# Performance work log

Hardware: AMD Instinct MI355X
Metric: run time of the kernel (lower is better)

Reference implementation:

```python
import jax, jax.numpy as jnp
import numpy as np

B, S, D, H, E, F = 4, 2048, 1024, 16, 8, 4096
CAP_FACTOR = 1.25
DH = D // H


def setup_inputs() -> dict:
    key = jax.random.key(0)
    ks = jax.random.split(key, 8)
    s = 0.02
    return {
        "src": jax.random.normal(ks[0], (B, S, D), jnp.float32),
        "src_pad_mask": jnp.zeros((B, S), jnp.bool_),  # True = padding
        "ln1_g": jnp.ones((D,), jnp.float32),
        "ln1_b": jnp.zeros((D,), jnp.float32),
        "in_proj_w": jax.random.normal(ks[1], (3 * D, D), jnp.float32) * s,
        "in_proj_b": jnp.zeros((3 * D,), jnp.float32),
        "out_proj_w": jax.random.normal(ks[2], (D, D), jnp.float32) * s,
        "out_proj_b": jnp.zeros((D,), jnp.float32),
        "ln2_g": jnp.ones((D,), jnp.float32),
        "ln2_b": jnp.zeros((D,), jnp.float32),
        "router_w": jax.random.normal(ks[3], (D, E), jnp.float32) * s,
        "router_b": jnp.zeros((E,), jnp.float32),
        "w1": jax.random.normal(ks[4], (E, D, F), jnp.float32) * s,
        "b1": jnp.zeros((E, F), jnp.float32),
        "w2": jax.random.normal(ks[5], (E, F, D), jnp.float32) * s,
        "b2": jnp.zeros((E, D), jnp.float32),
    }


def _layernorm(x, g, b, eps=1e-5):
    m = jnp.mean(x, axis=-1, keepdims=True)
    v = jnp.mean(jnp.square(x - m), axis=-1, keepdims=True)
    return (x - m) * jax.lax.rsqrt(v + eps) * g + b


def _mha(x, pad_mask, in_proj_w, in_proj_b, out_proj_w, out_proj_b):
    qkv = x @ in_proj_w.T + in_proj_b                      # [B,S,3D]
    q, k, v = jnp.split(qkv, 3, axis=-1)
    q = q.reshape(B, S, H, DH)
    k = k.reshape(B, S, H, DH)
    v = v.reshape(B, S, H, DH)
    scores = jnp.einsum('bqhd,bkhd->bhqk', q, k) / np.sqrt(DH).astype(np.float32)
    scores = jnp.where(pad_mask[:, None, None, :], jnp.float32(-1e9), scores)
    attn = jax.nn.softmax(scores, axis=-1)
    out = jnp.einsum('bhqk,bkhd->bqhd', attn, v).reshape(B, S, D)
    return out @ out_proj_w.T + out_proj_b


def _switch(x, token_mask, router_w, router_b, w1, b1, w2, b2):
    N = B * S
    cap = int(CAP_FACTOR * N / E)
    tokens = x.reshape(N, D)
    tm = token_mask.reshape(N).astype(jnp.float32)
    logits = tokens @ router_w + router_b                  # [N,E]
    probs = jax.nn.softmax(logits, axis=-1)
    eidx = jnp.argmax(probs, axis=-1)                      # [N] top-1 expert
    gate = jnp.take_along_axis(probs, eidx[:, None], axis=1)[:, 0]
    oh = jax.nn.one_hot(eidx, E, dtype=jnp.float32) * tm[:, None]
    # position of each token within its expert's queue (1-based; 0 if masked)
    pos = jnp.sum(jnp.cumsum(oh, axis=0) * oh, axis=-1)
    keep = (pos > 0) & (pos <= cap)
    slot = eidx * cap + (pos - 1).astype(jnp.int32)        # flat slot in [E*cap)
    slot_scatter = jnp.where(keep, slot, E * cap)          # out-of-range => dropped
    keepf = keep.astype(jnp.float32)
    dispatch = jnp.zeros((E * cap, D), jnp.float32).at[slot_scatter].set(
        tokens * keepf[:, None], mode='drop')
    d = dispatch.reshape(E, cap, D)
    h = jax.nn.relu(jnp.einsum('ecd,edf->ecf', d, w1) + b1[:, None, :])
    o = jnp.einsum('ecf,efd->ecd', h, w2) + b2[:, None, :]
    slot_gather = jnp.where(keep, slot, 0)
    out = o.reshape(E * cap, D)[slot_gather] * (gate * keepf)[:, None]
    # aux losses over valid tokens
    denom = jnp.maximum(jnp.sum(tm), 1.0)
    f = jnp.sum(oh, axis=0) / denom                        # dispatch fraction per expert
    P = jnp.sum(probs * tm[:, None], axis=0) / denom       # mean router prob per expert
    lb_loss = E * jnp.sum(f * P)
    z_loss = jnp.sum(jnp.square(jax.nn.logsumexp(logits, axis=-1)) * tm) / denom
    return out.reshape(B, S, D), lb_loss, z_loss


def reference(src, src_pad_mask, ln1_g, ln1_b, in_proj_w, in_proj_b,
              out_proj_w, out_proj_b, ln2_g, ln2_b, router_w, router_b,
              w1, b1, w2, b2):
    x = _layernorm(src, ln1_g, ln1_b)
    attn = _mha(x, src_pad_mask, in_proj_w, in_proj_b, out_proj_w, out_proj_b)
    src1 = src + attn                                      # dropout=0.0
    token_mask = ~src_pad_mask
    x2 = _layernorm(src1, ln2_g, ln2_b)
    ffn, lb_loss, z_loss = _switch(x2, token_mask, router_w, router_b, w1, b1, w2, b2)
    src2 = src1 + ffn
    return (src2, lb_loss, z_loss)
```

## Files before the change

kernel.cpp:

```cpp
#include <hip/hip_runtime.h>

constexpr int cB = 4, cS = 2048, cD = 1024, cH = 16, cE = 8, cF = 4096;
constexpr int cN = cB * cS;
constexpr int cDH = 64;
constexpr int cCAP = 1280;

typedef __attribute__((ext_vector_type(8))) short bf16x8;
typedef __attribute__((ext_vector_type(4))) float f32x4;
typedef __attribute__((ext_vector_type(4))) unsigned short u16x4;

__device__ inline unsigned short bf16_rne(float x) {
  unsigned u = __float_as_uint(x);
  u += 0x7FFF + ((u >> 16) & 1);
  return (unsigned short)(u >> 16);
}
__device__ inline float bf16_f(unsigned short h) {
  return __uint_as_float(((unsigned)h) << 16);
}

__global__ __launch_bounds__(256) void ln_kernel(const float* __restrict__ x,
                                                 const float* __restrict__ g,
                                                 const float* __restrict__ bb,
                                                 float* __restrict__ y) {
  __shared__ float red[8];
  const int row = blockIdx.x;
  const int t = threadIdx.x;
  const float4 v = ((const float4*)(x + (size_t)row * cD))[t];
  float s = v.x + v.y + v.z + v.w;
#pragma unroll
  for (int m = 32; m >= 1; m >>= 1) s += __shfl_xor(s, m, 64);
  if ((t & 63) == 0) red[t >> 6] = s;
  __syncthreads();
  const float mean = (red[0] + red[1] + red[2] + red[3]) * (1.0f / cD);
  const float dx = v.x - mean, dy = v.y - mean, dz = v.z - mean, dw = v.w - mean;
  float ss = dx * dx + dy * dy + dz * dz + dw * dw;
#pragma unroll
  for (int m = 32; m >= 1; m >>= 1) ss += __shfl_xor(ss, m, 64);
  if ((t & 63) == 0) red[4 + (t >> 6)] = ss;
  __syncthreads();
  const float var = (red[4] + red[5] + red[6] + red[7]) * (1.0f / cD);
  const float inv = rsqrtf(var + 1e-5f);
  const float4 gg = ((const float4*)g)[t];
  const float4 b4 = ((const float4*)bb)[t];
  float4 o;
  o.x = dx * inv * gg.x + b4.x;
  o.y = dy * inv * gg.y + b4.y;
  o.z = dz * inv * gg.z + b4.z;
  o.w = dw * inv * gg.w + b4.w;
  ((float4*)(y + (size_t)row * cD))[t] = o;
}

__global__ __launch_bounds__(256) void ln_split_kernel(
    const float* __restrict__ x, const float* __restrict__ g,
    const float* __restrict__ bb, unsigned short* __restrict__ yh,
    unsigned short* __restrict__ yl) {
  __shared__ float red[8];
  const int row = blockIdx.x;
  const int t = threadIdx.x;
  const float4 v = ((const float4*)(x + (size_t)row * cD))[t];
  float s = v.x + v.y + v.z + v.w;
#pragma unroll
  for (int m = 32; m >= 1; m >>= 1) s += __shfl_xor(s, m, 64);
  if ((t & 63) == 0) red[t >> 6] = s;
  __syncthreads();
  const float mean = (red[0] + red[1] + red[2] + red[3]) * (1.0f / cD);
  const float dx = v.x - mean, dy = v.y - mean, dz = v.z - mean, dw = v.w - mean;
  float ss = dx * dx + dy * dy + dz * dz + dw * dw;
#pragma unroll
  for (int m = 32; m >= 1; m >>= 1) ss += __shfl_xor(ss, m, 64);
  if ((t & 63) == 0) red[4 + (t >> 6)] = ss;
  __syncthreads();
  const float var = (red[4] + red[5] + red[6] + red[7]) * (1.0f / cD);
  const float inv = rsqrtf(var + 1e-5f);
  const float4 gg = ((const float4*)g)[t];
  const float4 b4 = ((const float4*)bb)[t];
  const float oa[4] = {dx * inv * gg.x + b4.x, dy * inv * gg.y + b4.y,
                       dz * inv * gg.z + b4.z, dw * inv * gg.w + b4.w};
  u16x4 hh, ll;
#pragma unroll
  for (int i = 0; i < 4; i++) {
    const unsigned short h16 = bf16_rne(oa[i]);
    hh[i] = h16;
    ll[i] = bf16_rne(oa[i] - bf16_f(h16));
  }
  *(u16x4*)(yh + (size_t)row * cD + t * 4) = hh;
  *(u16x4*)(yl + (size_t)row * cD + t * 4) = ll;
}

__global__ __launch_bounds__(256) void wsplit_kernel(const float* __restrict__ in,
                                                     unsigned short* __restrict__ hi,
                                                     unsigned short* __restrict__ lo,
                                                     int n4) {
  const int i = blockIdx.x * 256 + threadIdx.x;
  if (i >= n4) return;
  const float4 v = ((const float4*)in)[i];
  const float a[4] = {v.x, v.y, v.z, v.w};
  u16x4 hh, ll;
#pragma unroll
  for (int j = 0; j < 4; j++) {
    const unsigned short h16 = bf16_rne(a[j]);
    hh[j] = h16;
    ll[j] = bf16_rne(a[j] - bf16_f(h16));
  }
  *(u16x4*)(hi + (size_t)i * 4) = hh;
  *(u16x4*)(lo + (size_t)i * 4) = ll;
}

__global__ __launch_bounds__(256) void transpose_bf16_kernel(
    const float* __restrict__ in, unsigned short* __restrict__ outp, int Rr,
    int Cc) {
  __shared__ float T[64][65];
  const int z = blockIdx.z;
  in += (size_t)z * Rr * Cc;
  outp += (size_t)z * Rr * Cc;
  const int c0 = blockIdx.x * 64, r0 = blockIdx.y * 64;
  const int tid = threadIdx.x;
#pragma unroll
  for (int u = 0; u < 4; u++) {
    const int a = tid + u * 256;
    const int r = a >> 4, c4 = (a & 15) << 2;
    const float4 v = *(const float4*)(in + (size_t)(r0 + r) * Cc + c0 + c4);
    T[r][c4 + 0] = v.x;
    T[r][c4 + 1] = v.y;
    T[r][c4 + 2] = v.z;
    T[r][c4 + 3] = v.w;
  }
  __syncthreads();
#pragma unroll
  for (int u = 0; u < 4; u++) {
    const int a = tid + u * 256;
    const int c = a >> 4, r4 = (a & 15) << 2;
    u16x4 o;
#pragma unroll
    for (int i = 0; i < 4; i++) o[i] = bf16_rne(T[r4 + i][c]);
    *(u16x4*)(outp + (size_t)(c0 + c) * Rr + r0 + r4) = o;
  }
}

template <bool SPLIT, bool RELU, bool RESID, int OUT>
__global__ __launch_bounds__(256) void gemm_bf16(
    const unsigned short* __restrict__ Ah, const unsigned short* __restrict__ Al,
    size_t sA,
    const unsigned short* __restrict__ Bh, const unsigned short* __restrict__ Bl,
    size_t sB,
    const float* __restrict__ bias, size_t sBias,
    const float* __restrict__ R,
    void* __restrict__ Cv, size_t sC,
    int K, int lda, int ldb, int ldc,
    unsigned short* __restrict__ Qh, unsigned short* __restrict__ Ql,
    unsigned short* __restrict__ Kh, unsigned short* __restrict__ Kl,
    unsigned short* __restrict__ Vth, unsigned short* __restrict__ Vtl) {
  __shared__ unsigned short AsH[128 * 40];
  __shared__ unsigned short BsH[128 * 40];
  __shared__ unsigned short AsL[SPLIT ? 128 * 40 : 8];
  __shared__ unsigned short BsL[SPLIT ? 128 * 40 : 8];
  const int z = blockIdx.z;
  Ah += (size_t)z * sA;
  Bh += (size_t)z * sB;
  if constexpr (SPLIT) {
    Al += (size_t)z * sA;
    Bl += (size_t)z * sB;
  }
  bias += (size_t)z * sBias;
  const int n0 = blockIdx.x * 128, m0 = blockIdx.y * 128;
  const int tid = threadIdx.x;
  const int wid = tid >> 6, lane = tid & 63;
  const int ln = lane & 15, quad = lane >> 4;
  const int wm = (wid >> 1) * 64, wn = (wid & 1) * 64;

  f32x4 acc[4][4];
#pragma unroll
  for (int i = 0; i < 4; i++)
#pragma unroll
    for (int j = 0; j < 4; j++) acc[i][j] = (f32x4){0.f, 0.f, 0.f, 0.f};

  for (int k0 = 0; k0 < K; k0 += 32) {
    __syncthreads();
#pragma unroll
    for (int u = 0; u < 2; u++) {
      const int c = tid + u * 256;
      const int row = c >> 2, ko = (c & 3) << 3;
      const int ld = row * 40 + ko;
      *(uint4*)&AsH[ld] = *(const uint4*)(Ah + (size_t)(m0 + row) * lda + k0 + ko);
      *(uint4*)&BsH[ld] = *(const uint4*)(Bh + (size_t)(n0 + row) * ldb + k0 + ko);
      if constexpr (SPLIT) {
        *(uint4*)&AsL[ld] = *(const uint4*)(Al + (size_t)(m0 + row) * lda + k0 + ko);
        *(uint4*)&BsL[ld] = *(const uint4*)(Bl + (size_t)(n0 + row) * ldb + k0 + ko);
      }
    }
    __syncthreads();
    bf16x8 bh[4], bl[4];
#pragma unroll
    for (int nt = 0; nt < 4; nt++) {
      bh[nt] = *(const bf16x8*)&BsH[(wn + nt * 16 + ln) * 40 + quad * 8];
      if constexpr (SPLIT)
        bl[nt] = *(const bf16x8*)&BsL[(wn + nt * 16 + ln) * 40 + quad * 8];
    }
#pragma unroll
    for (int mt = 0; mt < 4; mt++) {
      const bf16x8 ah = *(const bf16x8*)&AsH[(wm + mt * 16 + ln) * 40 + quad * 8];
      bf16x8 al;
      if constexpr (SPLIT)
        al = *(const bf16x8*)&AsL[(wm + mt * 16 + ln) * 40 + quad * 8];
#pragma unroll
      for (int nt = 0; nt < 4; nt++) {
        acc[mt][nt] =
            __builtin_amdgcn_mfma_f32_16x16x32_bf16(ah, bh[nt], acc[mt][nt], 0, 0, 0);
        if constexpr (SPLIT) {
          acc[mt][nt] =
              __builtin_amdgcn_mfma_f32_16x16x32_bf16(al, bh[nt], acc[mt][nt], 0, 0, 0);
          acc[mt][nt] =
              __builtin_amdgcn_mfma_f32_16x16x32_bf16(ah, bl[nt], acc[mt][nt], 0, 0, 0);
        }
      }
    }
  }
  if constexpr (OUT == 2) {
#pragma unroll
    for (int mt = 0; mt < 4; mt++) {
      const int row0 = m0 + wm + mt * 16 + quad * 4;
      const int b_ = row0 >> 11, s0_ = row0 & 2047;
      const size_t bbase = (size_t)b_ * cH * cS * cDH;
#pragma unroll
      for (int nt = 0; nt < 4; nt++) {
        const int col = n0 + wn + nt * 16 + ln;
        const float bv = bias[col];
        const int sec = col >> 10;
        const int f = col & 1023;
        const int hh = f >> 6, d = f & 63;
        const size_t bh_off = bbase + (size_t)hh * cS * cDH;
        float vals[4];
#pragma unroll
        for (int r = 0; r < 4; r++) vals[r] = acc[mt][nt][r] + bv;
        if (sec == 2) {
          u16x4 hi4, lo4;
#pragma unroll
          for (int r = 0; r < 4; r++) {
            const unsigned short h16 = bf16_rne(vals[r]);
            hi4[r] = h16;
            lo4[r] = bf16_rne(vals[r] - bf16_f(h16));
          }
          const size_t idx = bh_off + (size_t)d * cS + s0_;
          *(u16x4*)(Vth + idx) = hi4;
          *(u16x4*)(Vtl + idx) = lo4;
        } else {
          unsigned short* dsth = (sec == 0) ? Qh : Kh;
          unsigned short* dstl = (sec == 0) ? Ql : Kl;
#pragma unroll
          for (int r = 0; r < 4; r++) {
            const unsigned short h16 = bf16_rne(vals[r]);
            const size_t idx = bh_off + (size_t)(s0_ + r) * cDH + d;
            dsth[idx] = h16;
            dstl[idx] = bf16_rne(vals[r] - bf16_f(h16));
          }
        }
      }
    }
  } else {
    float* Cf = nullptr;
    unsigned short* Cb = nullptr;
    if constexpr (OUT == 1)
      Cb = (unsigned short*)Cv + (size_t)z * sC;
    else
      Cf = (float*)Cv + (size_t)z * sC;
#pragma unroll
    for (int mt = 0; mt < 4; mt++) {
#pragma unroll
      for (int nt = 0; nt < 4; nt++) {
        const int col = n0 + wn + nt * 16 + ln;
        const float bv = bias[col];
#pragma unroll
        for (int r = 0; r < 4; r++) {
          const int row = m0 + wm + mt * 16 + quad * 4 + r;
          float v = acc[mt][nt][r] + bv;
          if constexpr (RELU) v = fmaxf(v, 0.f);
          if constexpr (RESID) v += R[(size_t)row * ldc + col];
          if constexpr (OUT == 1)
            Cb[(size_t)row * ldc + col] = bf16_rne(v);
          else
            Cf[(size_t)row * ldc + col] = v;
        }
      }
    }
  }
}

__global__ __launch_bounds__(256) void attn_mfma_kernel(
    const unsigned short* __restrict__ Qh, const unsigned short* __restrict__ Ql,
    const unsigned short* __restrict__ Kh, const unsigned short* __restrict__ Kl,
    const unsigned short* __restrict__ Vth, const unsigned short* __restrict__ Vtl,
    const unsigned char* __restrict__ pad, unsigned short* __restrict__ Oh,
    unsigned short* __restrict__ Ol) {
  __shared__ unsigned short KsH[64 * 72];
  __shared__ unsigned short KsL[64 * 72];
  __shared__ unsigned short VsH[64 * 72];
  __shared__ unsigned short VsL[64 * 72];
  __shared__ unsigned short PsH[4 * 16 * 72];
  __shared__ unsigned short PsL[4 * 16 * 72];
  __shared__ float Mk[64];

  const int q0 = blockIdx.x << 6;
  const int h = blockIdx.y, b = blockIdx.z;
  const int tid = threadIdx.x;
  const int wid = tid >> 6, lane = tid & 63;
  const int ln = lane & 15, quad = lane >> 4;
  constexpr float SC2 = 0.125f * 1.4426950408889634f;

  const size_t bh = (size_t)(b * cH + h);
  const unsigned short* gKh = Kh + bh * cS * cDH;
  const unsigned short* gKl = Kl + bh * cS * cDH;
  const unsigned short* gVh = Vth + bh * cDH * cS;
  const unsigned short* gVl = Vtl + bh * cDH * cS;

  const size_t qbase = (bh * cS + q0 + wid * 16 + ln) * cDH;
  bf16x8 qh[2], ql[2];
#pragma unroll
  for (int ks = 0; ks < 2; ks++) {
    qh[ks] = *(const bf16x8*)(Qh + qbase + ks * 32 + quad * 8);
    ql[ks] = *(const bf16x8*)(Ql + qbase + ks * 32 + quad * 8);
  }

  f32x4 Oc[4];
#pragma unroll
  for (int dt = 0; dt < 4; dt++) Oc[dt] = (f32x4){0.f, 0.f, 0.f, 0.f};
  float mprev = -1e30f, lrun = 0.f;

  for (int kt = 0; kt < cS / 64; kt++) {
    const int k0 = kt << 6;
    __syncthreads();
#pragma unroll
    for (int u = 0; u < 2; u++) {
      const int a = tid + (u << 8);
      const int row = a >> 3, c8 = (a & 7) << 3;
      const int ld = row * 72 + c8;
      *(uint4*)&KsH[ld] = *(const uint4*)(gKh + (size_t)(k0 + row) * cDH + c8);
      *(uint4*)&KsL[ld] = *(const uint4*)(gKl + (size_t)(k0 + row) * cDH + c8);
      *(uint4*)&VsH[ld] = *(const uint4*)(gVh + (size_t)row * cS + k0 + c8);
      *(uint4*)&VsL[ld] = *(const uint4*)(gVl + (size_t)row * cS + k0 + c8);
    }
    if (tid < 64) Mk[tid] = pad[b * cS + k0 + tid] ? -1e30f : 0.0f;
    __syncthreads();

    float sf[4][4];
#pragma unroll
    for (int st = 0; st < 4; st++) {
      f32x4 acc = (f32x4){0.f, 0.f, 0.f, 0.f};
      const unsigned short* krH = &KsH[(st * 16 + ln) * 72];
      const unsigned short* krL = &KsL[(st * 16 + ln) * 72];
#pragma unroll
      for (int ks = 0; ks < 2; ks++) {
        const bf16x8 kh = *(const bf16x8*)(krH + ks * 32 + quad * 8);
        const bf16x8 kl = *(const bf16x8*)(krL + ks * 32 + quad * 8);
        acc = __builtin_amdgcn_mfma_f32_16x16x32_bf16(kh, qh[ks], acc, 0, 0, 0);
        acc = __builtin_amdgcn_mfma_f32_16x16x32_bf16(kl, qh[ks], acc, 0, 0, 0);
        acc = __builtin_amdgcn_mfma_f32_16x16x32_bf16(kh, ql[ks], acc, 0, 0, 0);
      }
      const float4 mkv = *(const float4*)&Mk[st * 16 + quad * 4];
      sf[st][0] = acc[0] * SC2 + mkv.x;
      sf[st][1] = acc[1] * SC2 + mkv.y;
      sf[st][2] = acc[2] * SC2 + mkv.z;
      sf[st][3] = acc[3] * SC2 + mkv.w;
    }
    float vm = -1e30f;
#pragma unroll
    for (int st = 0; st < 4; st++)
#pragma unroll
      for (int r = 0; r < 4; r++) vm = fmaxf(vm, sf[st][r]);
    vm = fmaxf(vm, __shfl_xor(vm, 16, 64));
    vm = fmaxf(vm, __shfl_xor(vm, 32, 64));
    const float mnew = fmaxf(mprev, vm);
    const float alpha = exp2f(mprev - mnew);
    float rs = 0.f;
    u16x4 phv[4], plv[4];
#pragma unroll
    for (int st = 0; st < 4; st++) {
#pragma unroll
      for (int r = 0; r < 4; r++) {
        const float p = exp2f(sf[st][r] - mnew);
        rs += p;
        const unsigned short h16 = bf16_rne(p);
        phv[st][r] = h16;
        plv[st][r] = bf16_rne(p - bf16_f(h16));
      }
    }
    rs += __shfl_xor(rs, 16, 64);
    rs += __shfl_xor(rs, 32, 64);
    lrun = lrun * alpha + rs;
    mprev = mnew;
#pragma unroll
    for (int dt = 0; dt < 4; dt++) {
      Oc[dt][0] *= alpha;
      Oc[dt][1] *= alpha;
      Oc[dt][2] *= alpha;
      Oc[dt][3] *= alpha;
    }
    const int pbase = wid * 1152 + ln * 72 + quad * 4;
#pragma unroll
    for (int st = 0; st < 4; st++) {
      *(u16x4*)&PsH[pbase + st * 16] = phv[st];
      *(u16x4*)&PsL[pbase + st * 16] = plv[st];
    }
    const unsigned short* pwH = PsH + wid * 1152 + ln * 72;
    const unsigned short* pwL = PsL + wid * 1152 + ln * 72;
#pragma unroll
    for (int dt = 0; dt < 4; dt++) {
      f32x4 acc = Oc[dt];
      const unsigned short* vrH = &VsH[(dt * 16 + ln) * 72];
      const unsigned short* vrL = &VsL[(dt * 16 + ln) * 72];
#pragma unroll
      for (int ks = 0; ks < 2; ks++) {
        const bf16x8 vh = *(const bf16x8*)(vrH + ks * 32 + quad * 8);
        const bf16x8 vl = *(const bf16x8*)(vrL + ks * 32 + quad * 8);
        const bf16x8 pbh = *(const bf16x8*)(pwH + ks * 32 + quad * 8);
        const bf16x8 pbl = *(const bf16x8*)(pwL + ks * 32 + quad * 8);
        acc = __builtin_amdgcn_mfma_f32_16x16x32_bf16(vh, pbh, acc, 0, 0, 0);
        acc = __builtin_amdgcn_mfma_f32_16x16x32_bf16(vh, pbl, acc, 0, 0, 0);
        acc = __builtin_amdgcn_mfma_f32_16x16x32_bf16(vl, pbh, acc, 0, 0, 0);
      }
      Oc[dt] = acc;
    }
  }
  const float inv = 1.0f / lrun;
  const int tok = b * cS + q0 + wid * 16 + ln;
#pragma unroll
  for (int dt = 0; dt < 4; dt++) {
    u16x4 oh4, ol4;
#pragma unroll
    for (int r = 0; r < 4; r++) {
      const float v = Oc[dt][r] * inv;
      const unsigned short h16 = bf16_rne(v);
      oh4[r] = h16;
      ol4[r] = bf16_rne(v - bf16_f(h16));
    }
    const size_t idx = (size_t)tok * cD + h * cDH + dt * 16 + quad * 4;
    *(u16x4*)(Oh + idx) = oh4;
    *(u16x4*)(Ol + idx) = ol4;
  }
}

__global__ __launch_bounds__(256) void router_kernel(
    const float* __restrict__ x2, const float* __restrict__ rw,
    const float* __restrict__ rb, const unsigned char* __restrict__ pad,
    float* __restrict__ gate, int* __restrict__ eidx, float* __restrict__ Psum,
    float* __restrict__ zsum) {
  __shared__ float Pacc[8];
  __shared__ float Zacc;
  if (threadIdx.x < 8) Pacc[threadIdx.x] = 0.f;
  if (threadIdx.x == 8) Zacc = 0.f;
  __syncthreads();
  const int tid = threadIdx.x, wid = tid >> 6, lane = tid & 63;
  const int e = lane & 7, dbase = lane >> 3;
  for (int tok = blockIdx.x * 4 + wid; tok < cN; tok += gridDim.x * 4) {
    const float* xr = x2 + (size_t)tok * cD;
    float partial = 0.f;
#pragma unroll 8
    for (int i = 0; i < cD / 8; i++) {
      const int d = dbase + i * 8;
      partial += xr[d] * rw[d * 8 + e];
    }
    partial += __shfl_xor(partial, 8, 64);
    partial += __shfl_xor(partial, 16, 64);
    partial += __shfl_xor(partial, 32, 64);
    const float logit = partial + rb[e];
    float mx = logit;
    mx = fmaxf(mx, __shfl_xor(mx, 1, 64));
    mx = fmaxf(mx, __shfl_xor(mx, 2, 64));
    mx = fmaxf(mx, __shfl_xor(mx, 4, 64));
    const float ex = __expf(logit - mx);
    float sm = ex;
    sm += __shfl_xor(sm, 1, 64);
    sm += __shfl_xor(sm, 2, 64);
    sm += __shfl_xor(sm, 4, 64);
    const float prob = ex / sm;
    float bv = logit;
    int bi = e;
#pragma unroll
    for (int m = 1; m < 8; m <<= 1) {
      const float ov = __shfl_xor(bv, m, 64);
      const int oi = __shfl_xor(bi, m, 64);
      if (ov > bv || (ov == bv && oi < bi)) {
        bv = ov;
        bi = oi;
      }
    }
    const float g = __shfl(prob, (lane & 0x38) | bi, 64);
    const bool valid = (pad[tok] == 0);
    if (lane == 0) {
      eidx[tok] = bi;
      gate[tok] = g;
    }
    if (valid) {
      if (lane < 8) atomicAdd(&Pacc[lane], prob);
      if (lane == 0) {
        const float lse = mx + logf(sm);
        atomicAdd(&Zacc, lse * lse);
      }
    }
  }
  __syncthreads();
  if (threadIdx.x < 8) atomicAdd(&Psum[threadIdx.x], Pacc[threadIdx.x]);
  if (threadIdx.x == 8) atomicAdd(zsum, Zacc);
}

__global__ __launch_bounds__(256) void scan_kernel(const int* __restrict__ eidx,
                                                   const unsigned char* __restrict__ pad,
                                                   int* __restrict__ slot,
                                                   int* __restrict__ counts) {
  __shared__ int cnt[256][8];
  const int t = threadIdx.x;
  int lc[8] = {0, 0, 0, 0, 0, 0, 0, 0};
  const int base = t * 32;
  for (int i = 0; i < 32; i++) {
    const int tok = base + i;
    if (!pad[tok]) lc[eidx[tok]]++;
  }
#pragma unroll
  for (int e2 = 0; e2 < 8; e2++) cnt[t][e2] = lc[e2];
  __syncthreads();
  if (t < 8) {
    int run = 0;
    for (int i = 0; i < 256; i++) {
      const int v = cnt[i][t];
      cnt[i][t] = run;
      run += v;
    }
    counts[t] = run;
  }
  __syncthreads();
  int off[8];
#pragma unroll
  for (int e2 = 0; e2 < 8; e2++) off[e2] = cnt[t][e2];
  for (int i = 0; i < 32; i++) {
    const int tok = base + i;
    if (!pad[tok]) {
      const int e2 = eidx[tok];
      const int p = off[e2]++;
      slot[tok] = (p < cCAP) ? (e2 * cCAP + p) : -1;
    } else {
      slot[tok] = -1;
    }
  }
}

__global__ __launch_bounds__(256) void dispatch_bf16_kernel(
    const float* __restrict__ x2, const int* __restrict__ slot,
    unsigned short* __restrict__ disp) {
  const int tok = blockIdx.x;
  const int s = slot[tok];
  if (s < 0) return;
  const float4 v = ((const float4*)(x2 + (size_t)tok * cD))[threadIdx.x];
  u16x4 o;
  o[0] = bf16_rne(v.x);
  o[1] = bf16_rne(v.y);
  o[2] = bf16_rne(v.z);
  o[3] = bf16_rne(v.w);
  *(u16x4*)(disp + (size_t)s * cD + threadIdx.x * 4) = o;
}

__global__ __launch_bounds__(256) void gather_kernel(const float* __restrict__ src1,
                                                     const float* __restrict__ o,
                                                     const int* __restrict__ slot,
                                                     const float* __restrict__ gate,
                                                     float* __restrict__ out) {
  const int tok = blockIdx.x;
  float4 r = ((const float4*)(src1 + (size_t)tok * cD))[threadIdx.x];
  const int s = slot[tok];
  if (s >= 0) {
    const float g = gate[tok];
    const float4 ov = ((const float4*)(o + (size_t)s * cD))[threadIdx.x];
    r.x += g * ov.x;
    r.y += g * ov.y;
    r.z += g * ov.z;
    r.w += g * ov.w;
  }
  ((float4*)(out + (size_t)tok * cD))[threadIdx.x] = r;
}

__global__ void loss_kernel(const int* __restrict__ counts,
                            const float* __restrict__ Psum,
                            const float* __restrict__ zsum,
                            float* __restrict__ out) {
  if (threadIdx.x == 0) {
    int tot = 0;
    for (int e2 = 0; e2 < 8; e2++) tot += counts[e2];
    const float denom = fmaxf((float)tot, 1.0f);
    float lp = 0.f;
    for (int e2 = 0; e2 < 8; e2++)
      lp += ((float)counts[e2] / denom) * (Psum[e2] / denom);
    out[0] = 8.0f * lp;
    out[1] = zsum[0] / denom;
  }
}

constexpr size_t OFF_A = 0;
constexpr size_t OFF_B = 25165824;
constexpr size_t OFF_XHL = 50331648;
constexpr size_t OFF_SRC1 = 58720256;
constexpr size_t OFF_X2O = 67108864;
constexpr size_t OFF_IPW = 77594624;
constexpr size_t OFF_OPW = 80740352;
constexpr size_t OFF_MISC = 81788928;

extern "C" void kernel_launch(void* const* d_in, const int* in_sizes, int n_in,
                              void* d_out, int out_size, void* d_ws, size_t ws_size,
                              hipStream_t stream) {
  (void)in_sizes; (void)n_in; (void)out_size; (void)ws_size;
  const float* src = (const float*)d_in[0];
  const unsigned char* pad = (const unsigned char*)d_in[1];
  const float* ln1_g = (const float*)d_in[2];
  const float* ln1_b = (const float*)d_in[3];
  const float* in_proj_w = (const float*)d_in[4];
  const float* in_proj_b = (const float*)d_in[5];
  const float* out_proj_w = (const float*)d_in[6];
  const float* out_proj_b = (const float*)d_in[7];
  const float* ln2_g = (const float*)d_in[8];
  const float* ln2_b = (const float*)d_in[9];
  const float* router_w = (const float*)d_in[10];
  const float* router_b = (const float*)d_in[11];
  const float* w1 = (const float*)d_in[12];
  const float* b1 = (const float*)d_in[13];
  const float* w2 = (const float*)d_in[14];
  const float* b2 = (const float*)d_in[15];
  float* out = (float*)d_out;
  float* w = (float*)d_ws;

  unsigned short* w1t = (unsigned short*)(w + OFF_A);
  unsigned short* w2t = (unsigned short*)(w + OFF_A);
  unsigned short* usB = (unsigned short*)(w + OFF_B);
  constexpr size_t SPN = (size_t)cN * cD;
  unsigned short* Qh = usB + 0 * SPN;
  unsigned short* Ql = usB + 1 * SPN;
  unsigned short* Kh = usB + 2 * SPN;
  unsigned short* Kl = usB + 3 * SPN;
  unsigned short* Vth = usB + 4 * SPN;
  unsigned short* Vtl = usB + 5 * SPN;
  unsigned short* hbuf16 = usB;
  unsigned short* xh = (unsigned short*)(w + OFF_XHL);
  unsigned short* xl = xh + SPN;
  unsigned short* Oh = xh;
  unsigned short* Ol = xh + SPN;
  unsigned short* disp16 = xh;
  float* src1 = w + OFF_SRC1;
  float* x2 = w + OFF_X2O;
  float* obuf = w + OFF_X2O;
  unsigned short* ipwh = (unsigned short*)(w + OFF_IPW);
  unsigned short* ipwl = ipwh + (size_t)3 * cD * cD;
  unsigned short* opwh = (unsigned short*)(w + OFF_OPW);
  unsigned short* opwl = opwh + (size_t)cD * cD;
  float* gate = w + OFF_MISC;
  int* eidx = (int*)(w + OFF_MISC + 8192);
  int* slot = (int*)(w + OFF_MISC + 16384);
  float* Psum = w + OFF_MISC + 24576;
  float* zsum = Psum + 8;
  int* counts = (int*)(Psum + 16);

  hipMemsetAsync(Psum, 0, 9 * sizeof(float), stream);

  ln_split_kernel<<<cN, 256, 0, stream>>>(src, ln1_g, ln1_b, xh, xl);
  wsplit_kernel<<<3072, 256, 0, stream>>>(in_proj_w, ipwh, ipwl, 786432);
  wsplit_kernel<<<1024, 256, 0, stream>>>(out_proj_w, opwh, opwl, 262144);
  gemm_bf16<true, false, false, 2><<<dim3(24, 64, 1), 256, 0, stream>>>(
      xh, xl, 0, ipwh, ipwl, 0, in_proj_b, 0, nullptr, nullptr, 0,
      cD, cD, cD, 0, Qh, Ql, Kh, Kl, Vth, Vtl);
  transpose_bf16_kernel<<<dim3(64, 16, 8), 256, 0, stream>>>(w1, w1t, cD, cF);
  attn_mfma_kernel<<<dim3(cS / 64, cH, cB), 256, 0, stream>>>(
      Qh, Ql, Kh, Kl, Vth, Vtl, pad, Oh, Ol);
  gemm_bf16<true, false, true, 0><<<dim3(8, 64, 1), 256, 0, stream>>>(
      Oh, Ol, 0, opwh, opwl, 0, out_proj_b, 0, src, src1, 0,
      cD, cD, cD, cD, nullptr, nullptr, nullptr, nullptr, nullptr, nullptr);
  ln_kernel<<<cN, 256, 0, stream>>>(src1, ln2_g, ln2_b, x2);
  router_kernel<<<256, 256, 0, stream>>>(x2, router_w, router_b, pad, gate, eidx,
                                         Psum, zsum);
  scan_kernel<<<1, 256, 0, stream>>>(eidx, pad, slot, counts);
  dispatch_bf16_kernel<<<cN, 256, 0, stream>>>(x2, slot, disp16);
  gemm_bf16<false, true, false, 1><<<dim3(32, 10, 8), 256, 0, stream>>>(
      disp16, nullptr, (size_t)cCAP * cD, w1t, nullptr, (size_t)cD * cF,
      b1, cF, nullptr, hbuf16, (size_t)cCAP * cF, cD, cD, cD, cF,
      nullptr, nullptr, nullptr, nullptr, nullptr, nullptr);
  transpose_bf16_kernel<<<dim3(16, 64, 8), 256, 0, stream>>>(w2, w2t, cF, cD);
  gemm_bf16<false, false, false, 0><<<dim3(8, 10, 8), 256, 0, stream>>>(
      hbuf16, nullptr, (size_t)cCAP * cF, w2t, nullptr, (size_t)cF * cD,
      b2, cD, nullptr, obuf, (size_t)cCAP * cD, cF, cF, cF, cD,
      nullptr, nullptr, nullptr, nullptr, nullptr, nullptr);
  gather_kernel<<<cN, 256, 0, stream>>>(src1, obuf, slot, gate, out);
  loss_kernel<<<1, 64, 0, stream>>>(counts, Psum, zsum, out + (size_t)cN * cD);
}
```

Measured before the change: 1.411 ms.

## Drop LDS staging in attention; load K/V straight from global into registers

The attention kernel stops staging K, V and the mask through shared memory and removes both per-tile barriers. Each wave now reads its K rows and V-transposed fragments directly from global memory, and P is kept in registers in the MFMA B-operand layout instead of being round-tripped through LDS. A small new kernel precomputes the padding mask as floats so the kernel can read it with vector loads. This removes LDS traffic and synchronisation, but each of the four waves now issues its own redundant global/L2 loads of the same K/V tile, and the V loads are narrower 8-byte reads.

Result: slower. 2.371 ms (+68.0%).

```diff
diff --git a/kernel.cpp b/kernel.cpp
--- a/kernel.cpp
+++ b/kernel.cpp
@@ -104,6 +104,12 @@
   }
   *(u16x4*)(hi + (size_t)i * 4) = hh;
   *(u16x4*)(lo + (size_t)i * 4) = ll;
+}
+
+__global__ __launch_bounds__(256) void padmask_kernel(
+    const unsigned char* __restrict__ pad, float* __restrict__ mkf) {
+  const int i = blockIdx.x * 256 + threadIdx.x;
+  mkf[i] = pad[i] ? -1e30f : 0.0f;
 }
 
 __global__ __launch_bounds__(256) void transpose_bf16_kernel(
@@ -285,20 +291,19 @@
   }
 }
 
+__device__ inline bf16x8 cat44(const u16x4 a, const u16x4 b) {
+  bf16x8 r;
+  r[0] = (short)a[0]; r[1] = (short)a[1]; r[2] = (short)a[2]; r[3] = (short)a[3];
+  r[4] = (short)b[0]; r[5] = (short)b[1]; r[6] = (short)b[2]; r[7] = (short)b[3];
+  return r;
+}
+
 __global__ __launch_bounds__(256) void attn_mfma_kernel(
     const unsigned short* __restrict__ Qh, const unsigned short* __restrict__ Ql,
     const unsigned short* __restrict__ Kh, const unsigned short* __restrict__ Kl,
     const unsigned short* __restrict__ Vth, const unsigned short* __restrict__ Vtl,
-    const unsigned char* __restrict__ pad, unsigned short* __restrict__ Oh,
+    const float* __restrict__ mkf, unsigned short* __restrict__ Oh,
     unsigned short* __restrict__ Ol) {
-  __shared__ unsigned short KsH[64 * 72];
-  __shared__ unsigned short KsL[64 * 72];
-  __shared__ unsigned short VsH[64 * 72];
-  __shared__ unsigned short VsL[64 * 72];
-  __shared__ unsigned short PsH[4 * 16 * 72];
-  __shared__ unsigned short PsL[4 * 16 * 72];
-  __shared__ float Mk[64];
-
   const int q0 = blockIdx.x << 6;
   const int h = blockIdx.y, b = blockIdx.z;
   const int tid = threadIdx.x;
@@ -311,6 +316,7 @@
   const unsigned short* gKl = Kl + bh * cS * cDH;
   const unsigned short* gVh = Vth + bh * cDH * cS;
   const unsigned short* gVl = Vtl + bh * cDH * cS;
+  const float* gM = mkf + (size_t)b * cS;
 
   const size_t qbase = (bh * cS + q0 + wid * 16 + ln) * cDH;
   bf16x8 qh[2], ql[2];
@@ -327,35 +333,21 @@
 
   for (int kt = 0; kt < cS / 64; kt++) {
     const int k0 = kt << 6;
-    __syncthreads();
-#pragma unroll
-    for (int u = 0; u < 2; u++) {
-      const int a = tid + (u << 8);
-      const int row = a >> 3, c8 = (a & 7) << 3;
-      const int ld = row * 72 + c8;
-      *(uint4*)&KsH[ld] = *(const uint4*)(gKh + (size_t)(k0 + row) * cDH + c8);
-      *(uint4*)&KsL[ld] = *(const uint4*)(gKl + (size_t)(k0 + row) * cDH + c8);
-      *(uint4*)&VsH[ld] = *(const uint4*)(gVh + (size_t)row * cS + k0 + c8);
-      *(uint4*)&VsL[ld] = *(const uint4*)(gVl + (size_t)row * cS + k0 + c8);
-    }
-    if (tid < 64) Mk[tid] = pad[b * cS + k0 + tid] ? -1e30f : 0.0f;
-    __syncthreads();
-
     float sf[4][4];
 #pragma unroll
     for (int st = 0; st < 4; st++) {
       f32x4 acc = (f32x4){0.f, 0.f, 0.f, 0.f};
-      const unsigned short* krH = &KsH[(st * 16 + ln) * 72];
-      const unsigned short* krL = &KsL[(st * 16 + ln) * 72];
+      const unsigned short* krH = gKh + (size_t)(k0 + st * 16 + ln) * cDH + quad * 8;
+      const unsigned short* krL = gKl + (size_t)(k0 + st * 16 + ln) * cDH + quad * 8;
 #pragma unroll
       for (int ks = 0; ks < 2; ks++) {
-        const bf16x8 kh = *(const bf16x8*)(krH + ks * 32 + quad * 8);
-        const bf16x8 kl = *(const bf16x8*)(krL + ks * 32 + quad * 8);
+        const bf16x8 kh = *(const bf16x8*)(krH + ks * 32);
+        const bf16x8 kl = *(const bf16x8*)(krL + ks * 32);
         acc = __builtin_amdgcn_mfma_f32_16x16x32_bf16(kh, qh[ks], acc, 0, 0, 0);
         acc = __builtin_amdgcn_mfma_f32_16x16x32_bf16(kl, qh[ks], acc, 0, 0, 0);
         acc = __builtin_amdgcn_mfma_f32_16x16x32_bf16(kh, ql[ks], acc, 0, 0, 0);
       }
-      const float4 mkv = *(const float4*)&Mk[st * 16 + quad * 4];
+      const float4 mkv = *(const float4*)(gM + k0 + st * 16 + quad * 4);
       sf[st][0] = acc[0] * SC2 + mkv.x;
       sf[st][1] = acc[1] * SC2 + mkv.y;
       sf[st][2] = acc[2] * SC2 + mkv.z;
@@ -371,7 +363,7 @@
     const float mnew = fmaxf(mprev, vm);
     const float alpha = exp2f(mprev - mnew);
     float rs = 0.f;
-    u16x4 phv[4], plv[4];
+    bf16x8 pbh[2], pbl[2];
 #pragma unroll
     for (int st = 0; st < 4; st++) {
 #pragma unroll
@@ -379,8 +371,8 @@
         const float p = exp2f(sf[st][r] - mnew);
         rs += p;
         const unsigned short h16 = bf16_rne(p);
-        phv[st][r] = h16;
-        plv[st][r] = bf16_rne(p - bf16_f(h16));
+        pbh[st >> 1][(st & 1) * 4 + r] = (short)h16;
+        pbl[st >> 1][(st & 1) * 4 + r] = (short)bf16_rne(p - bf16_f(h16));
       }
     }
     rs += __shfl_xor(rs, 16, 64);
@@ -394,28 +386,20 @@
       Oc[dt][2] *= alpha;
       Oc[dt][3] *= alpha;
     }
-    const int pbase = wid * 1152 + ln * 72 + quad * 4;
-#pragma unroll
-    for (int st = 0; st < 4; st++) {
-      *(u16x4*)&PsH[pbase + st * 16] = phv[st];
-      *(u16x4*)&PsL[pbase + st * 16] = plv[st];
-    }
-    const unsigned short* pwH = PsH + wid * 1152 + ln * 72;
-    const unsigned short* pwL = PsL + wid * 1152 + ln * 72;
 #pragma unroll
     for (int dt = 0; dt < 4; dt++) {
       f32x4 acc = Oc[dt];
-      const unsigned short* vrH = &VsH[(dt * 16 + ln) * 72];
-      const unsigned short* vrL = &VsL[(dt * 16 + ln) * 72];
+      const unsigned short* vrH = gVh + (size_t)(dt * 16 + ln) * cS + k0 + quad * 4;
+      const unsigned short* vrL = gVl + (size_t)(dt * 16 + ln) * cS + k0 + quad * 4;
 #pragma unroll
       for (int ks = 0; ks < 2; ks++) {
-        const bf16x8 vh = *(const bf16x8*)(vrH + ks * 32 + quad * 8);
-        const bf16x8 vl = *(const bf16x8*)(vrL + ks * 32 + quad * 8);
-        const bf16x8 pbh = *(const bf16x8*)(pwH + ks * 32 + quad * 8);
-        const bf16x8 pbl = *(const bf16x8*)(pwL + ks * 32 + quad * 8);
-        acc = __builtin_amdgcn_mfma_f32_16x16x32_bf16(vh, pbh, acc, 0, 0, 0);
-        acc = __builtin_amdgcn_mfma_f32_16x16x32_bf16(vh, pbl, acc, 0, 0, 0);
-        acc = __builtin_amdgcn_mfma_f32_16x16x32_bf16(vl, pbh, acc, 0, 0, 0);
+        const bf16x8 vh = cat44(*(const u16x4*)(vrH + ks * 32),
+                                *(const u16x4*)(vrH + ks * 32 + 16));
+        const bf16x8 vl = cat44(*(const u16x4*)(vrL + ks * 32),
+                                *(const u16x4*)(vrL + ks * 32 + 16));
+        acc = __builtin_amdgcn_mfma_f32_16x16x32_bf16(vh, pbh[ks], acc, 0, 0, 0);
+        acc = __builtin_amdgcn_mfma_f32_16x16x32_bf16(vh, pbl[ks], acc, 0, 0, 0);
+        acc = __builtin_amdgcn_mfma_f32_16x16x32_bf16(vl, pbh[ks], acc, 0, 0, 0);
       }
       Oc[dt] = acc;
     }
@@ -641,6 +625,7 @@
   unsigned short* Ol = xh + SPN;
   unsigned short* disp16 = xh;
   float* src1 = w + OFF_SRC1;
+  float* mkf = w + OFF_X2O;
   float* x2 = w + OFF_X2O;
   float* obuf = w + OFF_X2O;
   unsigned short* ipwh = (unsigned short*)(w + OFF_IPW);
@@ -657,6 +642,7 @@
   hipMemsetAsync(Psum, 0, 9 * sizeof(float), stream);
 
   ln_split_kernel<<<cN, 256, 0, stream>>>(src, ln1_g, ln1_b, xh, xl);
+  padmask_kernel<<<cN / 256, 256, 0, stream>>>(pad, mkf);
   wsplit_kernel<<<3072, 256, 0, stream>>>(in_proj_w, ipwh, ipwl, 786432);
   wsplit_kernel<<<1024, 256, 0, stream>>>(out_proj_w, opwh, opwl, 262144);
   gemm_bf16<true, false, false, 2><<<dim3(24, 64, 1), 256, 0, stream>>>(
@@ -664,7 +650,7 @@
       cD, cD, cD, 0, Qh, Ql, Kh, Kl, Vth, Vtl);
   transpose_bf16_kernel<<<dim3(64, 16, 8), 256, 0, stream>>>(w1, w1t, cD, cF);
   attn_mfma_kernel<<<dim3(cS / 64, cH, cB), 256, 0, stream>>>(
-      Qh, Ql, Kh, Kl, Vth, Vtl, pad, Oh, Ol);
+      Qh, Ql, Kh, Kl, Vth, Vtl, mkf, Oh, Ol);
   gemm_bf16<true, false, true, 0><<<dim3(8, 64, 1), 256, 0, stream>>>(
       Oh, Ol, 0, opwh, opwl, 0, out_proj_b, 0, src, src1, 0,
       cD, cD, cD, cD, nullptr, nullptr, nullptr, nullptr, nullptr, nullptr);
```
